# Performance work log

Hardware: AMD Instinct MI355X
Metric: run time of the kernel (lower is better)

The kernel has to match this reference:

```python
import jax, jax.numpy as jnp
import numpy as np

B, T, E, H = 8, 2048, 256, 8
D = E // H  # head_size = 32
EPS = 1e-5  # torch LayerNorm default


def _layernorm(x, g, b):
    m = jnp.mean(x, axis=-1, keepdims=True)
    v = jnp.var(x, axis=-1, keepdims=True)
    return (x - m) / jnp.sqrt(v + EPS) * g + b


def setup_inputs() -> dict:
    key = jax.random.key(0)
    ks = jax.random.split(key, 9)
    s = lambda k, shape, fan: (jax.random.normal(k, shape, jnp.float32) / np.sqrt(fan)).astype(jnp.float32)
    return {
        "x": jax.random.normal(ks[0], (B, T, E), jnp.float32),
        "wq": s(ks[1], (H, E, D), E),
        "wk": s(ks[2], (H, E, D), E),
        "wv": s(ks[3], (H, E, D), E),
        "w_lin": s(ks[4], (E, E), E),
        "b_lin": jnp.zeros((E,), jnp.float32),
        "g1": jnp.ones((E,), jnp.float32),
        "beta1": jnp.zeros((E,), jnp.float32),
        "g2": jnp.ones((E,), jnp.float32),
        "beta2": jnp.zeros((E,), jnp.float32),
        "w_f1": s(ks[5], (E, 4 * E), E),
        "b_f1": jnp.zeros((4 * E,), jnp.float32),
        "w_f2": s(ks[6], (4 * E, E), 4 * E),
        "b_f2": jnp.zeros((E,), jnp.float32),
    }


def reference(x, wq, wk, wv, w_lin, b_lin, g1, beta1, g2, beta2, w_f1, b_f1, w_f2, b_f2):
    b, t, e = x.shape
    xn = _layernorm(x, g1, beta1)  # norm1
    # all heads at once: (B,T,E) x (H,E,D) -> (B,H,T,D)
    q = jnp.einsum('bte,hed->bhtd', xn, wq)
    k = jnp.einsum('bte,hed->bhtd', xn, wk)
    v = jnp.einsum('bte,hed->bhtd', xn, wv)
    # scale uses C = embedding_size (as in source, not head_size)
    scores = jnp.einsum('bhtd,bhsd->bhts', q, k) * (e ** -0.5)
    mask = jnp.tril(jnp.ones((t, t), bool))  # (query t, key s)
    scores = jnp.where(mask[None, None, :, :], scores, -jnp.inf)
    # source applies softmax over dim=1 of (B,T,T) = the QUERY axis -> axis 2 of bhts
    attn = jax.nn.softmax(scores, axis=2)
    heads = jnp.einsum('bhts,bhsd->bhtd', attn, v)
    heads = heads.transpose(0, 2, 1, 3).reshape(b, t, e)  # concat over heads
    xh = xn + heads  # residual around attention
    xl = xh @ w_lin + b_lin  # projection (dropout is identity at eval)
    x2 = _layernorm(xl, g2, beta2)  # norm2
    ff = jax.nn.relu(x2 @ w_f1 + b_f1) @ w_f2 + b_f2  # FFN (dropout identity)
    return x2 + ff
```

## Files before the change

### kernel.cpp

```cpp
#include <hip/hip_runtime.h>
#include <math.h>

#define TT 2048
#define TE 256
#define NTOK 16384
#define QSCALE (0.0625f * 1.44269504088896f)

typedef short  bf16x8 __attribute__((ext_vector_type(8)));
typedef float  f32x4  __attribute__((ext_vector_type(4)));
typedef float  f32x16 __attribute__((ext_vector_type(16)));
typedef unsigned short u16x4 __attribute__((ext_vector_type(4)));
typedef unsigned short u16x8 __attribute__((ext_vector_type(8)));

__device__ __forceinline__ unsigned short f2b(float f) {
    union { float f; unsigned int u; } v; v.f = f;
    unsigned int r = v.u + 0x7FFF + ((v.u >> 16) & 1);
    return (unsigned short)(r >> 16);
}
__device__ __forceinline__ float b2f(unsigned short u) {
    union { unsigned int i; float f; } v; v.i = ((unsigned int)u) << 16;
    return v.f;
}
#if __has_builtin(__builtin_amdgcn_cvt_pk_bf16_f32)
__device__ __forceinline__ unsigned int pk_bf16(float a, float b) {
    typedef __bf16 bf2 __attribute__((ext_vector_type(2)));
    union { bf2 v; unsigned int u; } u;
    u.v = __builtin_amdgcn_cvt_pk_bf16_f32(a, b);
    return u.u;
}
#else
__device__ __forceinline__ unsigned int pk_bf16(float a, float b) {
    return (unsigned int)f2b(a) | ((unsigned int)f2b(b) << 16);
}
#endif
#if __has_builtin(__builtin_amdgcn_exp2f)
#define FEXP2(x) __builtin_amdgcn_exp2f(x)
#else
#define FEXP2(x) __expf(0.69314718056f * (x))
#endif
__device__ __forceinline__ void pswap(unsigned &a, unsigned &b) {
#if __has_builtin(__builtin_amdgcn_permlane32_swap)
    auto r = __builtin_amdgcn_permlane32_swap(a, b, false, false);
    a = r[0]; b = r[1];
#else
    asm("v_permlane32_swap_b32 %0, %1" : "+v"(a), "+v"(b));
#endif
}
__device__ __forceinline__ bf16x8 ld8(const unsigned short* p) {
    return *(const bf16x8*)p;
}
__device__ __forceinline__ void gl_lds16(const unsigned short* g, unsigned short* l) {
    __builtin_amdgcn_global_load_lds(
        (const __attribute__((address_space(1))) unsigned int*)(uintptr_t)g,
        (__attribute__((address_space(3))) unsigned int*)(uintptr_t)l,
        16, 0, 0);
}
#define MFMA16(a, b, c) __builtin_amdgcn_mfma_f32_16x16x32_bf16((a), (b), (c), 0, 0, 0)
#define MFMA32(a, b, c) __builtin_amdgcn_mfma_f32_32x32x16_bf16((a), (b), (c), 0, 0, 0)


__global__ __launch_bounds__(256) void conv_w(const float* __restrict__ wq,
                                              const float* __restrict__ wk,
                                              const float* __restrict__ wv,
                                              const float* __restrict__ w_lin,
                                              const float* __restrict__ w_f1,
                                              const float* __restrict__ w_f2,
                                              unsigned short* __restrict__ Wqkv,
                                              unsigned short* __restrict__ Wlin,
                                              unsigned short* __restrict__ Wf1,
                                              unsigned short* __restrict__ Wf2) {
    int idx = blockIdx.x * 256 + threadIdx.x;
    if (idx < 196608) {
        int n = idx >> 8, k = idx & 255;
        int which = n >> 8, h = (n >> 5) & 7, d = n & 31;
        const float* w = (which == 0) ? wq : (which == 1) ? wk : wv;
        Wqkv[idx] = f2b(w[(h * 256 + k) * 32 + d]);
    } else if (idx < 262144) {
        int i = idx - 196608; int n = i >> 8, k = i & 255;
        Wlin[i] = f2b(w_lin[k * 256 + n]);
    } else if (idx < 524288) {
        int i = idx - 262144; int n = i >> 8, k = i & 255;
        Wf1[i] = f2b(w_f1[k * 1024 + n]);
    } else {
        int i = idx - 524288; int n = i >> 10, k = i & 1023;
        Wf2[i] = f2b(w_f2[k * 256 + n]);
    }
}

__global__ __launch_bounds__(256) void ln_w(const float* __restrict__ X,
                                            const float* __restrict__ g,
                                            const float* __restrict__ bta,
                                            float* __restrict__ Y,
                                            unsigned short* __restrict__ Yb) {
    int row = blockIdx.x * 4 + (threadIdx.x >> 6);
    int lane = threadIdx.x & 63;
    const float4 v = *(const float4*)&X[(size_t)row * TE + lane * 4];
    float s = v.x + v.y + v.z + v.w;
    float s2 = v.x * v.x + v.y * v.y + v.z * v.z + v.w * v.w;
#pragma unroll
    for (int off = 1; off <= 32; off <<= 1) {
        s  += __shfl_xor(s,  off, 64);
        s2 += __shfl_xor(s2, off, 64);
    }
    float mean = s * (1.0f / TE);
    float var = s2 * (1.0f / TE) - mean * mean;
    float rstd = rsqrtf(var + 1e-5f);
    const float4 gg = *(const float4*)&g[lane * 4];
    const float4 bb = *(const float4*)&bta[lane * 4];
    float4 o;
    o.x = (v.x - mean) * rstd * gg.x + bb.x;
    o.y = (v.y - mean) * rstd * gg.y + bb.y;
    o.z = (v.z - mean) * rstd * gg.z + bb.z;
    o.w = (v.w - mean) * rstd * gg.w + bb.w;
    if (Y) *(float4*)&Y[(size_t)row * TE + lane * 4] = o;
    if (Yb) {
        u16x4 ob = { f2b(o.x), f2b(o.y), f2b(o.z), f2b(o.w) };
        *(u16x4*)&Yb[(size_t)row * TE + lane * 4] = ob;
    }
}

__global__ __launch_bounds__(256) void ln2_red(const float* __restrict__ Pp,
                                               const float* __restrict__ bias,
                                               const float* __restrict__ g,
                                               const float* __restrict__ bta,
                                               unsigned short* __restrict__ Yb) {
    const size_t SL = (size_t)NTOK * TE;
    int row = blockIdx.x * 4 + (threadIdx.x >> 6);
    int lane = threadIdx.x & 63;
    size_t base = (size_t)row * TE + lane * 4;
    const float4 p0 = *(const float4*)&Pp[base];
    const float4 p1 = *(const float4*)&Pp[SL + base];
    const float4 bl = *(const float4*)&bias[lane * 4];
    float4 v;
    v.x = p0.x + p1.x + bl.x; v.y = p0.y + p1.y + bl.y;
    v.z = p0.z + p1.z + bl.z; v.w = p0.w + p1.w + bl.w;
    float s = v.x + v.y + v.z + v.w;
    float s2 = v.x * v.x + v.y * v.y + v.z * v.z + v.w * v.w;
#pragma unroll
    for (int off = 1; off <= 32; off <<= 1) {
        s  += __shfl_xor(s,  off, 64);
        s2 += __shfl_xor(s2, off, 64);
    }
    float mean = s * (1.0f / TE);
    float var = s2 * (1.0f / TE) - mean * mean;
    float rstd = rsqrtf(var + 1e-5f);
    const float4 gg = *(const float4*)&g[lane * 4];
    const float4 bb = *(const float4*)&bta[lane * 4];
    u16x4 ob = { f2b((v.x - mean) * rstd * gg.x + bb.x),
                 f2b((v.y - mean) * rstd * gg.y + bb.y),
                 f2b((v.z - mean) * rstd * gg.z + bb.z),
                 f2b((v.w - mean) * rstd * gg.w + bb.w) };
    *(u16x4*)&Yb[base] = ob;
}

__global__ __launch_bounds__(256) void reduce2(const unsigned short* __restrict__ Pf,
                                               const float* __restrict__ bias,
                                               const unsigned short* __restrict__ x2b,
                                               float* __restrict__ out) {
    const size_t SL = (size_t)NTOK * TE;
    int row = blockIdx.x * 4 + (threadIdx.x >> 6);
    int lane = threadIdx.x & 63;
    size_t base = (size_t)row * TE + lane * 4;
    const float4 bl = *(const float4*)&bias[lane * 4];
    u16x4 r = *(const u16x4*)&x2b[base];
    float4 acc;
    acc.x = bl.x + b2f(r[0]); acc.y = bl.y + b2f(r[1]);
    acc.z = bl.z + b2f(r[2]); acc.w = bl.w + b2f(r[3]);
#pragma unroll
    for (int z = 0; z < 4; ++z) {
        u16x4 p = *(const u16x4*)&Pf[z * SL + base];
        acc.x += b2f(p[0]); acc.y += b2f(p[1]);
        acc.z += b2f(p[2]); acc.w += b2f(p[3]);
    }
    *(float4*)&out[base] = acc;
}

template<int KS>
__global__ __launch_bounds__(256) void gemm_lds(const unsigned short* __restrict__ A,
                                                int lda,
                                                const unsigned short* __restrict__ Bt,
                                                int ldb,
                                                const float* __restrict__ bias,
                                                float* __restrict__ outF,
                                                unsigned short* __restrict__ outB,
                                                int N, int relu) {
    __shared__ unsigned short Al[2][128 * 32];
    __shared__ unsigned short Bl[2][128 * 32];
    int tid = threadIdx.x;
    int w = tid >> 6, lane = tid & 63, q = lane >> 4, col = lane & 15;
    int wm = w & 1, wn = w >> 1;
    int m0 = blockIdx.x * 128;
    int n0 = blockIdx.y * 128;
    int koff = blockIdx.z * KS;
    size_t zoff = (size_t)blockIdx.z * NTOK * N;
    f32x4 acc[4][4] = {};
    int srow = lane >> 2;
    int skq  = ((lane & 3) ^ ((srow >> 1) & 3)) * 8;
    const unsigned short* Ag0 = A  + (size_t)(m0 + w * 32 + srow) * lda + koff + skq;
    const unsigned short* Ag1 = Ag0 + (size_t)16 * lda;
    const unsigned short* Bg0 = Bt + (size_t)(n0 + w * 32 + srow) * ldb + koff + skq;
    const unsigned short* Bg1 = Bg0 + (size_t)16 * ldb;
    int rq = (q ^ ((col >> 1) & 3)) * 8;
#define G_STAGE(cur, k0) do { \
        gl_lds16(Ag0 + (k0), &Al[cur][(w * 32) * 32]); \
        gl_lds16(Ag1 + (k0), &Al[cur][(w * 32 + 16) * 32]); \
        gl_lds16(Bg0 + (k0), &Bl[cur][(w * 32) * 32]); \
        gl_lds16(Bg1 + (k0), &Bl[cur][(w * 32 + 16) * 32]); \
    } while (0)
    G_STAGE(0, 0);
    __syncthreads();
    int cur = 0;
#pragma unroll
    for (int k0 = 0; k0 < KS; k0 += 32) {
        int kn = k0 + 32;
        if (kn < KS) G_STAGE(cur ^ 1, kn);
        bf16x8 a[4], b[4];
#pragma unroll
        for (int i = 0; i < 4; ++i)
            a[i] = ld8(&Al[cur][(wm * 64 + i * 16 + col) * 32 + rq]);
#pragma unroll
        for (int j = 0; j < 4; ++j)
            b[j] = ld8(&Bl[cur][(wn * 64 + j * 16 + col) * 32 + rq]);
#pragma unroll
        for (int i = 0; i < 4; ++i)
#pragma unroll
            for (int j = 0; j < 4; ++j)
                acc[i][j] = MFMA16(a[i], b[j], acc[i][j]);
        if (kn < KS) { __syncthreads(); cur ^= 1; }
    }
#undef G_STAGE
#pragma unroll
    for (int i = 0; i < 4; ++i)
#pragma unroll
    for (int j = 0; j < 4; ++j) {
        int n = n0 + wn * 64 + j * 16 + col;
#pragma unroll
        for (int r = 0; r < 4; ++r) {
            int m = m0 + wm * 64 + i * 16 + q * 4 + r;
            float v = acc[i][j][r];
            if (bias) v += bias[n];
            if (relu) v = fmaxf(v, 0.f);
            if (outF) outF[zoff + (size_t)m * N + n] = v;
            if (outB) outB[zoff + (size_t)m * N + n] = f2b(v);
        }
    }
}

__global__ __launch_bounds__(256) void gemm_qkv(const unsigned short* __restrict__ A,
                                                const unsigned short* __restrict__ Bt,
                                                unsigned short* __restrict__ Qd,
                                                unsigned short* __restrict__ Kd,
                                                unsigned short* __restrict__ Vc) {
    const int K = 256;
    __shared__ unsigned short Al[2][128 * 32];
    __shared__ unsigned short Bl[2][128 * 32];
    int tid = threadIdx.x;
    int w = tid >> 6, lane = tid & 63, q = lane >> 4, col = lane & 15;
    int wm = w & 1, wn = w >> 1;
    int m0 = blockIdx.x * 128;
    int n0 = blockIdx.y * 128;
    f32x4 acc[4][4] = {};
    int srow = lane >> 2;
    int skq  = ((lane & 3) ^ ((srow >> 1) & 3)) * 8;
    const unsigned short* Ag0 = A  + (size_t)(m0 + w * 32 + srow) * K + skq;
    const unsigned short* Ag1 = Ag0 + (size_t)16 * K;
    const unsigned short* Bg0 = Bt + (size_t)(n0 + w * 32 + srow) * K + skq;
    const unsigned short* Bg1 = Bg0 + (size_t)16 * K;
    int rq = (q ^ ((col >> 1) & 3)) * 8;
#define G_STAGE(cur, k0) do { \
        gl_lds16(Ag0 + (k0), &Al[cur][(w * 32) * 32]); \
        gl_lds16(Ag1 + (k0), &Al[cur][(w * 32 + 16) * 32]); \
        gl_lds16(Bg0 + (k0), &Bl[cur][(w * 32) * 32]); \
        gl_lds16(Bg1 + (k0), &Bl[cur][(w * 32 + 16) * 32]); \
    } while (0)
    G_STAGE(0, 0);
    __syncthreads();
    int cur = 0;
#pragma unroll
    for (int k0 = 0; k0 < K; k0 += 32) {
        int kn = k0 + 32;
        if (kn < K) G_STAGE(cur ^ 1, kn);
        bf16x8 a[4], b[4];
#pragma unroll
        for (int i = 0; i < 4; ++i)
            a[i] = ld8(&Al[cur][(wm * 64 + i * 16 + col) * 32 + rq]);
#pragma unroll
        for (int j = 0; j < 4; ++j)
            b[j] = ld8(&Bl[cur][(wn * 64 + j * 16 + col) * 32 + rq]);
#pragma unroll
        for (int i = 0; i < 4; ++i)
#pragma unroll
            for (int j = 0; j < 4; ++j)
                acc[i][j] = MFMA16(a[i], b[j], acc[i][j]);
        if (kn < K) { __syncthreads(); cur ^= 1; }
    }
#undef G_STAGE
#pragma unroll
    for (int i = 0; i < 4; ++i)
#pragma unroll
    for (int j = 0; j < 4; ++j) {
        int n = n0 + wn * 64 + j * 16 + col;
        int which = n >> 8, h = (n >> 5) & 7, d = n & 31;
        int m = m0 + wm * 64 + i * 16 + q * 4;
        int b = m >> 11, t = m & 2047;
        int bh = b * 8 + h;
        if (which == 0) {
            size_t qb = ((size_t)(bh * 2 + (d >> 4)) * TT + t) * 16 + (d & 15);
#pragma unroll
            for (int r = 0; r < 4; ++r)
                Qd[qb + r * 16] = f2b(acc[i][j][r] * QSCALE);
        } else if (which == 1) {
            size_t kb = ((size_t)(bh * 2 + (d >> 4)) * TT + t) * 16 + (d & 15);
#pragma unroll
            for (int r = 0; r < 4; ++r)
                Kd[kb + r * 16] = f2b(acc[i][j][r]);
        } else {
            uint2 pv;
            pv.x = pk_bf16(acc[i][j][0], acc[i][j][1]);
            pv.y = pk_bf16(acc[i][j][2], acc[i][j][3]);
            *(uint2*)&Vc[(((size_t)bh * 256 + (t >> 3)) * 32 + d) * 8 + (t & 7)] = pv;
        }
    }
}

__global__ __launch_bounds__(256, 4) void attn_cols(const unsigned short* __restrict__ Qd,
                                                    const unsigned short* __restrict__ Kd,
                                                    float* __restrict__ colLinv) {
    __shared__ float Lb[4][32];
    int tid = threadIdx.x;
    int w = tid >> 6, lane = tid & 63, hi = lane >> 5, l31 = lane & 31;
    int bh = blockIdx.x;
    int u = blockIdx.y;
    const unsigned short* Qb = Qd + ((size_t)bh * 2 * TT + l31) * 16 + hi * 8;
    const unsigned short* Kb = Kd + ((size_t)bh * 2 * TT + l31) * 16 + hi * 8;
    const f32x16 z16 = {};
#pragma unroll
    for (int phase = 0; phase < 2; ++phase) {
        int stile = phase ? (63 - u) : u;
        int sbase = stile * 32;
        bf16x8 a0 = ld8(Kb + (size_t)sbase * 16);
        bf16x8 a1 = ld8(Kb + ((size_t)TT + sbase) * 16);
        float acc[16] = {};
        for (int ct = stile + w; ct < 64; ct += 4) {
            int t0 = ct * 32;
            bf16x8 q0 = ld8(Qb + (size_t)t0 * 16);
            bf16x8 q1 = ld8(Qb + ((size_t)TT + t0) * 16);
            f32x16 st = MFMA32(a0, q0, z16);
            st = MFMA32(a1, q1, st);
            if (ct == stile) {
#pragma unroll
                for (int r = 0; r < 16; ++r) {
                    int s_local = (r & 3) + 8 * (r >> 2) + 4 * hi;
                    acc[r] += (l31 >= s_local) ? FEXP2(st[r]) : 0.f;
                }
            } else {
#pragma unroll
                for (int r = 0; r < 16; ++r) acc[r] += FEXP2(st[r]);
            }
        }
#pragma unroll
        for (int off = 1; off <= 16; off <<= 1)
#pragma unroll
            for (int r = 0; r < 16; ++r) acc[r] += __shfl_xor(acc[r], off, 64);
        if (l31 == 0) {
#pragma unroll
            for (int r = 0; r < 16; ++r) {
                int s_local = (r & 3) + 8 * (r >> 2) + 4 * hi;
                Lb[w][s_local] = acc[r];
            }
        }
        __syncthreads();
        if (tid < 32) {
            float s = Lb[0][tid] + Lb[1][tid] + Lb[2][tid] + Lb[3][tid];
            colLinv[(size_t)bh * TT + sbase + tid] = 1.0f / s;
        }
        __syncthreads();
    }
}

__global__ __launch_bounds__(256) void scale_vt(unsigned short* __restrict__ Vc,
                                                const float* __restrict__ colLinv) {
    int bh = blockIdx.x >> 5, g = blockIdx.x & 31;
    int sb = g * 8 + (threadIdx.x >> 5);
    int d = threadIdx.x & 31;
    size_t base = (((size_t)bh * 256 + sb) * 32 + d) * 8;
    u16x8 v = *(const u16x8*)&Vc[base];
    const float4 i0 = *(const float4*)&colLinv[(size_t)bh * TT + sb * 8];
    const float4 i1 = *(const float4*)&colLinv[(size_t)bh * TT + sb * 8 + 4];
    u16x8 o;
    o[0] = f2b(b2f(v[0]) * i0.x); o[1] = f2b(b2f(v[1]) * i0.y);
    o[2] = f2b(b2f(v[2]) * i0.z); o[3] = f2b(b2f(v[3]) * i0.w);
    o[4] = f2b(b2f(v[4]) * i1.x); o[5] = f2b(b2f(v[5]) * i1.y);
    o[6] = f2b(b2f(v[6]) * i1.z); o[7] = f2b(b2f(v[7]) * i1.w);
    *(u16x8*)&Vc[base] = o;
}

__global__ __launch_bounds__(256, 4) void attn_out(const unsigned short* __restrict__ Qd,
                                                   const unsigned short* __restrict__ Kd,
                                                   const unsigned short* __restrict__ Vc,
                                                   const unsigned short* __restrict__ xnb,
                                                   unsigned short* __restrict__ xh_bf) {
    __shared__ float Ob[4][32][36];
    int tid = threadIdx.x;
    int w = tid >> 6, lane = tid & 63, hi = lane >> 5, l31 = lane & 31;
    int bh = blockIdx.x, b = bh >> 3, h = bh & 7;
    int u = blockIdx.y;
    const unsigned short* Kb = Kd + ((size_t)bh * 2 * TT + l31) * 16 + hi * 8;
    const unsigned short* Vb = Vc + (size_t)bh * 65536 + hi * 256 + l31 * 8;
    const unsigned short* Qbase = Qd + ((size_t)bh * 2 * TT + l31) * 16 + hi * 8;
    const f32x16 z16 = {};

#pragma unroll
    for (int phase = 0; phase < 2; ++phase) {
        int tt = phase ? (63 - u) : u;
        int tbase = tt * 32;
        bf16x8 q0 = ld8(Qbase + (size_t)tbase * 16);
        bf16x8 q1 = ld8(Qbase + ((size_t)TT + tbase) * 16);
        f32x16 acc = z16;

        int c = w;
        bf16x8 ka0 = ld8(Kb + (size_t)c * 512);
        bf16x8 ka1 = ld8(Kb + (size_t)TT * 16 + (size_t)c * 512);
        bf16x8 vv0 = ld8(Vb + (size_t)c * 1024);
        bf16x8 vv1 = ld8(Vb + (size_t)c * 1024 + 512);

        for (; c <= tt; c += 4) {
            bool diag = (c == tt);
            f32x16 st = MFMA32(ka0, q0, z16);
            st = MFMA32(ka1, q1, st);
            int cn = c + 4;
            if (cn <= tt) {
                ka0 = ld8(Kb + (size_t)cn * 512);
                ka1 = ld8(Kb + (size_t)TT * 16 + (size_t)cn * 512);
            }
            unsigned Wd[8];
            if (diag) {
#pragma unroll
                for (int j = 0; j < 8; ++j) {
                    int r0 = 2 * j;
                    int s0 = (r0 & 3) + 8 * (r0 >> 2) + 4 * hi;
                    float e0 = (s0 <= l31)     ? FEXP2(st[r0])     : 0.f;
                    float e1 = (s0 + 1 <= l31) ? FEXP2(st[r0 + 1]) : 0.f;
                    Wd[j] = pk_bf16(e0, e1);
                }
            } else {
#pragma unroll
                for (int j = 0; j < 8; ++j)
                    Wd[j] = pk_bf16(FEXP2(st[2 * j]), FEXP2(st[2 * j + 1]));
            }
            pswap(Wd[0], Wd[2]); pswap(Wd[1], Wd[3]);
            pswap(Wd[4], Wd[6]); pswap(Wd[5], Wd[7]);
            union { unsigned u4[4]; bf16x8 v; } pa0, pa1;
            pa0.u4[0] = Wd[0]; pa0.u4[1] = Wd[1]; pa0.u4[2] = Wd[2]; pa0.u4[3] = Wd[3];
            pa1.u4[0] = Wd[4]; pa1.u4[1] = Wd[5]; pa1.u4[2] = Wd[6]; pa1.u4[3] = Wd[7];
            acc = MFMA32(pa0.v, vv0, acc);
            acc = MFMA32(pa1.v, vv1, acc);
            if (cn <= tt) {
                vv0 = ld8(Vb + (size_t)cn * 1024);
                vv1 = ld8(Vb + (size_t)cn * 1024 + 512);
            }
        }

#pragma unroll
        for (int r = 0; r < 16; ++r) {
            int t = (r & 3) + 8 * (r >> 2) + 4 * hi;
            Ob[w][t][l31] = acc[r];
        }
        __syncthreads();
        {
            int row = tid >> 3;
            int c4 = (tid & 7) * 4;
            float4 s0 = *(const float4*)&Ob[0][row][c4];
            float4 s1 = *(const float4*)&Ob[1][row][c4];
            float4 s2 = *(const float4*)&Ob[2][row][c4];
            float4 s3 = *(const float4*)&Ob[3][row][c4];
            size_t base = ((size_t)(b * TT) + tbase + row) * TE + h * 32 + c4;
            u16x4 xv = *(const u16x4*)&xnb[base];
            u16x4 ob = { f2b(s0.x + s1.x + s2.x + s3.x + b2f(xv[0])),
                         f2b(s0.y + s1.y + s2.y + s3.y + b2f(xv[1])),
                         f2b(s0.z + s1.z + s2.z + s3.z + b2f(xv[2])),
                         f2b(s0.w + s1.w + s2.w + s3.w + b2f(xv[3])) };
            *(u16x4*)&xh_bf[base] = ob;
        }
        __syncthreads();
    }
}

extern "C" void kernel_launch(void* const* d_in, const int* in_sizes, int n_in,
                              void* d_out, int out_size, void* d_ws, size_t ws_size,
                              hipStream_t stream) {
    (void)in_sizes; (void)n_in; (void)out_size; (void)ws_size;
    const float* x     = (const float*)d_in[0];
    const float* wq    = (const float*)d_in[1];
    const float* wk    = (const float*)d_in[2];
    const float* wv    = (const float*)d_in[3];
    const float* w_lin = (const float*)d_in[4];
    const float* b_lin = (const float*)d_in[5];
    const float* g1    = (const float*)d_in[6];
    const float* beta1 = (const float*)d_in[7];
    const float* g2    = (const float*)d_in[8];
    const float* beta2 = (const float*)d_in[9];
    const float* w_f1  = (const float*)d_in[10];
    const float* b_f1  = (const float*)d_in[11];
    const float* w_f2  = (const float*)d_in[12];
    const float* b_f2  = (const float*)d_in[13];
    float* out = (float*)d_out;

    char* ws = (char*)d_ws;
    unsigned short* Wqkv_t = (unsigned short*)(ws + 0);
    unsigned short* Wlin_t = (unsigned short*)(ws + 393216);
    unsigned short* Wf1_t  = (unsigned short*)(ws + 524288);
    unsigned short* Wf2_t  = (unsigned short*)(ws + 1048576);
    float*          colLinv= (float*)(ws + 1572864);
    unsigned short* xn_bf  = (unsigned short*)(ws + 2097152);
    unsigned short* Qbf    = (unsigned short*)(ws + 10485760);
    unsigned short* Kbf    = (unsigned short*)(ws + 18874368);
    unsigned short* Vt     = (unsigned short*)(ws + 27262976);
    unsigned short* xh_bf  = (unsigned short*)(ws + 35651584);
    float*          Pp     = (float*)(ws + 44040192);
    unsigned short* Pf     = (unsigned short*)(ws + 44040192);
    unsigned short* x2_bf  = xn_bf;
    unsigned short* h_bf   = Qbf;

    conv_w<<<3072, 256, 0, stream>>>(wq, wk, wv, w_lin, w_f1, w_f2,
                                     Wqkv_t, Wlin_t, Wf1_t, Wf2_t);
    ln_w<<<4096, 256, 0, stream>>>(x, g1, beta1, nullptr, xn_bf);
    gemm_qkv<<<dim3(128, 6), 256, 0, stream>>>(xn_bf, Wqkv_t, Qbf, Kbf, Vt);
    attn_cols<<<dim3(64, 32), 256, 0, stream>>>(Qbf, Kbf, colLinv);
    scale_vt<<<2048, 256, 0, stream>>>(Vt, colLinv);
    attn_out<<<dim3(64, 32), 256, 0, stream>>>(Qbf, Kbf, Vt, xn_bf, xh_bf);
    gemm_lds<128><<<dim3(128, 2, 2), 256, 0, stream>>>(xh_bf, 256, Wlin_t, 256,
                                                       nullptr, Pp, nullptr, 256, 0);
    ln2_red<<<4096, 256, 0, stream>>>(Pp, b_lin, g2, beta2, x2_bf);
    gemm_lds<256><<<dim3(128, 8, 1), 256, 0, stream>>>(x2_bf, 256, Wf1_t, 256,
                                                       b_f1, nullptr, h_bf, 1024, 1);
    gemm_lds<256><<<dim3(128, 2, 4), 256, 0, stream>>>(h_bf, 1024, Wf2_t, 1024,
                                                       nullptr, nullptr, Pf, 256, 0);
    reduce2<<<4096, 256, 0, stream>>>(Pf, b_f2, x2_bf, out);
}
```

Baseline: 262.8 us.

## Fuse prep kernels, fold V scaling into attn_cols, triple-buffer GEMMs, stage epilogue

Merges weight conversion and the first LayerNorm into one launch, and folds the per-column V scaling into attn_cols so the scale_vt kernel and the colLinv buffer go away. The GEMM main loops move from double to triple-buffered LDS with explicit vmcnt waits and a single barrier per step. The gemm_lds epilogue is staged through LDS so outputs go out as vector stores. This cuts launch count and intermediate traffic and improves load/compute overlap, at the cost of more LDS per block and hand-written wait counts that rely on the number of outstanding loads being exact.

```diff
diff --git a/kernel.cpp b/kernel.cpp
--- a/kernel.cpp
+++ b/kernel.cpp
@@ -59,16 +59,43 @@
 #define MFMA32(a, b, c) __builtin_amdgcn_mfma_f32_32x32x16_bf16((a), (b), (c), 0, 0, 0)
 
 
-__global__ __launch_bounds__(256) void conv_w(const float* __restrict__ wq,
-                                              const float* __restrict__ wk,
-                                              const float* __restrict__ wv,
-                                              const float* __restrict__ w_lin,
-                                              const float* __restrict__ w_f1,
-                                              const float* __restrict__ w_f2,
-                                              unsigned short* __restrict__ Wqkv,
-                                              unsigned short* __restrict__ Wlin,
-                                              unsigned short* __restrict__ Wf1,
-                                              unsigned short* __restrict__ Wf2) {
+__global__ __launch_bounds__(256) void prep(const float* __restrict__ wq,
+                                            const float* __restrict__ wk,
+                                            const float* __restrict__ wv,
+                                            const float* __restrict__ w_lin,
+                                            const float* __restrict__ w_f1,
+                                            const float* __restrict__ w_f2,
+                                            unsigned short* __restrict__ Wqkv,
+                                            unsigned short* __restrict__ Wlin,
+                                            unsigned short* __restrict__ Wf1,
+                                            unsigned short* __restrict__ Wf2,
+                                            const float* __restrict__ X,
+                                            const float* __restrict__ g,
+                                            const float* __restrict__ bta,
+                                            unsigned short* __restrict__ Yb) {
+    if (blockIdx.x >= 3072) {
+        int row = (blockIdx.x - 3072) * 4 + (threadIdx.x >> 6);
+        int lane = threadIdx.x & 63;
+        const float4 v = *(const float4*)&X[(size_t)row * TE + lane * 4];
+        float s = v.x + v.y + v.z + v.w;
+        float s2 = v.x * v.x + v.y * v.y + v.z * v.z + v.w * v.w;
+#pragma unroll
+        for (int off = 1; off <= 32; off <<= 1) {
+            s  += __shfl_xor(s,  off, 64);
+            s2 += __shfl_xor(s2, off, 64);
+        }
+        float mean = s * (1.0f / TE);
+        float var = s2 * (1.0f / TE) - mean * mean;
+        float rstd = rsqrtf(var + 1e-5f);
+        const float4 gg = *(const float4*)&g[lane * 4];
+        const float4 bb = *(const float4*)&bta[lane * 4];
+        u16x4 ob = { f2b((v.x - mean) * rstd * gg.x + bb.x),
+                     f2b((v.y - mean) * rstd * gg.y + bb.y),
+                     f2b((v.z - mean) * rstd * gg.z + bb.z),
+                     f2b((v.w - mean) * rstd * gg.w + bb.w) };
+        *(u16x4*)&Yb[(size_t)row * TE + lane * 4] = ob;
+        return;
+    }
     int idx = blockIdx.x * 256 + threadIdx.x;
     if (idx < 196608) {
         int n = idx >> 8, k = idx & 255;
@@ -84,38 +111,6 @@
     } else {
         int i = idx - 524288; int n = i >> 10, k = i & 1023;
         Wf2[i] = f2b(w_f2[k * 256 + n]);
-    }
-}
-
-__global__ __launch_bounds__(256) void ln_w(const float* __restrict__ X,
-                                            const float* __restrict__ g,
-                                            const float* __restrict__ bta,
-                                            float* __restrict__ Y,
-                                            unsigned short* __restrict__ Yb) {
-    int row = blockIdx.x * 4 + (threadIdx.x >> 6);
-    int lane = threadIdx.x & 63;
-    const float4 v = *(const float4*)&X[(size_t)row * TE + lane * 4];
-    float s = v.x + v.y + v.z + v.w;
-    float s2 = v.x * v.x + v.y * v.y + v.z * v.z + v.w * v.w;
-#pragma unroll
-    for (int off = 1; off <= 32; off <<= 1) {
-        s  += __shfl_xor(s,  off, 64);
-        s2 += __shfl_xor(s2, off, 64);
-    }
-    float mean = s * (1.0f / TE);
-    float var = s2 * (1.0f / TE) - mean * mean;
-    float rstd = rsqrtf(var + 1e-5f);
-    const float4 gg = *(const float4*)&g[lane * 4];
-    const float4 bb = *(const float4*)&bta[lane * 4];
-    float4 o;
-    o.x = (v.x - mean) * rstd * gg.x + bb.x;
-    o.y = (v.y - mean) * rstd * gg.y + bb.y;
-    o.z = (v.z - mean) * rstd * gg.z + bb.z;
-    o.w = (v.w - mean) * rstd * gg.w + bb.w;
-    if (Y) *(float4*)&Y[(size_t)row * TE + lane * 4] = o;
-    if (Yb) {
-        u16x4 ob = { f2b(o.x), f2b(o.y), f2b(o.z), f2b(o.w) };
-        *(u16x4*)&Yb[(size_t)row * TE + lane * 4] = ob;
     }
 }
 
@@ -184,8 +179,8 @@
                                                 float* __restrict__ outF,
                                                 unsigned short* __restrict__ outB,
                                                 int N, int relu) {
-    __shared__ unsigned short Al[2][128 * 32];
-    __shared__ unsigned short Bl[2][128 * 32];
+    __shared__ unsigned short Al[3][128 * 32];
+    __shared__ unsigned short Bl[3][128 * 32];
     int tid = threadIdx.x;
     int w = tid >> 6, lane = tid & 63, q = lane >> 4, col = lane & 15;
     int wm = w & 1, wn = w >> 1;
@@ -201,47 +196,78 @@
     const unsigned short* Bg0 = Bt + (size_t)(n0 + w * 32 + srow) * ldb + koff + skq;
     const unsigned short* Bg1 = Bg0 + (size_t)16 * ldb;
     int rq = (q ^ ((col >> 1) & 3)) * 8;
-#define G_STAGE(cur, k0) do { \
-        gl_lds16(Ag0 + (k0), &Al[cur][(w * 32) * 32]); \
-        gl_lds16(Ag1 + (k0), &Al[cur][(w * 32 + 16) * 32]); \
-        gl_lds16(Bg0 + (k0), &Bl[cur][(w * 32) * 32]); \
-        gl_lds16(Bg1 + (k0), &Bl[cur][(w * 32 + 16) * 32]); \
+#define G_STAGE(bf, kk) do { \
+        gl_lds16(Ag0 + (kk), &Al[bf][(w * 32) * 32]); \
+        gl_lds16(Ag1 + (kk), &Al[bf][(w * 32 + 16) * 32]); \
+        gl_lds16(Bg0 + (kk), &Bl[bf][(w * 32) * 32]); \
+        gl_lds16(Bg1 + (kk), &Bl[bf][(w * 32 + 16) * 32]); \
     } while (0)
     G_STAGE(0, 0);
-    __syncthreads();
-    int cur = 0;
+    G_STAGE(1, 32);
 #pragma unroll
     for (int k0 = 0; k0 < KS; k0 += 32) {
-        int kn = k0 + 32;
-        if (kn < KS) G_STAGE(cur ^ 1, kn);
+        const int jb = (k0 >> 5) % 3;
+        if (k0 + 32 < KS) { asm volatile("s_waitcnt vmcnt(4)" ::: "memory"); }
+        else              { asm volatile("s_waitcnt vmcnt(0)" ::: "memory"); }
+        __builtin_amdgcn_s_barrier();
+        if (k0 + 64 < KS) G_STAGE((jb + 2) % 3, k0 + 64);
         bf16x8 a[4], b[4];
 #pragma unroll
         for (int i = 0; i < 4; ++i)
-            a[i] = ld8(&Al[cur][(wm * 64 + i * 16 + col) * 32 + rq]);
+            a[i] = ld8(&Al[jb][(wm * 64 + i * 16 + col) * 32 + rq]);
 #pragma unroll
         for (int j = 0; j < 4; ++j)
-            b[j] = ld8(&Bl[cur][(wn * 64 + j * 16 + col) * 32 + rq]);
+            b[j] = ld8(&Bl[jb][(wn * 64 + j * 16 + col) * 32 + rq]);
 #pragma unroll
         for (int i = 0; i < 4; ++i)
 #pragma unroll
             for (int j = 0; j < 4; ++j)
                 acc[i][j] = MFMA16(a[i], b[j], acc[i][j]);
-        if (kn < KS) { __syncthreads(); cur ^= 1; }
+        __builtin_amdgcn_sched_barrier(0);
     }
 #undef G_STAGE
-#pragma unroll
-    for (int i = 0; i < 4; ++i)
-#pragma unroll
-    for (int j = 0; j < 4; ++j) {
-        int n = n0 + wn * 64 + j * 16 + col;
-#pragma unroll
-        for (int r = 0; r < 4; ++r) {
-            int m = m0 + wm * 64 + i * 16 + q * 4 + r;
-            float v = acc[i][j][r];
-            if (bias) v += bias[n];
-            if (relu) v = fmaxf(v, 0.f);
-            if (outF) outF[zoff + (size_t)m * N + n] = v;
-            if (outB) outB[zoff + (size_t)m * N + n] = f2b(v);
+    float* Cb = (float*)&Al[0][0];
+    const int CLD = 132;
+#pragma unroll
+    for (int i = 0; i < 4; ++i) {
+        __syncthreads();
+#pragma unroll
+        for (int j = 0; j < 4; ++j)
+#pragma unroll
+            for (int r = 0; r < 4; ++r)
+                Cb[(wm * 16 + q * 4 + r) * CLD + wn * 64 + j * 16 + col] = acc[i][j][r];
+        __syncthreads();
+        int row = tid >> 3;
+        int seg = (tid & 7) * 16;
+        int mloc = (row & 15) + i * 16 + (row >> 4) * 64;
+        int m = m0 + mloc;
+        int n = n0 + seg;
+        float vbuf[16];
+#pragma unroll
+        for (int u = 0; u < 16; ++u) vbuf[u] = Cb[row * CLD + seg + u];
+        if (bias) {
+#pragma unroll
+            for (int u4 = 0; u4 < 4; ++u4) {
+                float4 bb = *(const float4*)&bias[n + u4 * 4];
+                vbuf[u4 * 4 + 0] += bb.x; vbuf[u4 * 4 + 1] += bb.y;
+                vbuf[u4 * 4 + 2] += bb.z; vbuf[u4 * 4 + 3] += bb.w;
+            }
+        }
+        if (relu) {
+#pragma unroll
+            for (int u = 0; u < 16; ++u) vbuf[u] = fmaxf(vbuf[u], 0.f);
+        }
+        if (outF) {
+#pragma unroll
+            for (int u = 0; u < 16; u += 4)
+                *(float4*)&outF[zoff + (size_t)m * N + n + u] = *(const float4*)&vbuf[u];
+        }
+        if (outB) {
+            u16x8 o0, o1;
+#pragma unroll
+            for (int u = 0; u < 8; ++u) { o0[u] = f2b(vbuf[u]); o1[u] = f2b(vbuf[8 + u]); }
+            *(u16x8*)&outB[zoff + (size_t)m * N + n] = o0;
+            *(u16x8*)&outB[zoff + (size_t)m * N + n + 8] = o1;
         }
     }
 }
@@ -252,8 +278,8 @@
                                                 unsigned short* __restrict__ Kd,
                                                 unsigned short* __restrict__ Vc) {
     const int K = 256;
-    __shared__ unsigned short Al[2][128 * 32];
-    __shared__ unsigned short Bl[2][128 * 32];
+    __shared__ unsigned short Al[3][128 * 32];
+    __shared__ unsigned short Bl[3][128 * 32];
     int tid = threadIdx.x;
     int w = tid >> 6, lane = tid & 63, q = lane >> 4, col = lane & 15;
     int wm = w & 1, wn = w >> 1;
@@ -267,32 +293,34 @@
     const unsigned short* Bg0 = Bt + (size_t)(n0 + w * 32 + srow) * K + skq;
     const unsigned short* Bg1 = Bg0 + (size_t)16 * K;
     int rq = (q ^ ((col >> 1) & 3)) * 8;
-#define G_STAGE(cur, k0) do { \
-        gl_lds16(Ag0 + (k0), &Al[cur][(w * 32) * 32]); \
-        gl_lds16(Ag1 + (k0), &Al[cur][(w * 32 + 16) * 32]); \
-        gl_lds16(Bg0 + (k0), &Bl[cur][(w * 32) * 32]); \
-        gl_lds16(Bg1 + (k0), &Bl[cur][(w * 32 + 16) * 32]); \
+#define G_STAGE(bf, kk) do { \
+        gl_lds16(Ag0 + (kk), &Al[bf][(w * 32) * 32]); \
+        gl_lds16(Ag1 + (kk), &Al[bf][(w * 32 + 16) * 32]); \
+        gl_lds16(Bg0 + (kk), &Bl[bf][(w * 32) * 32]); \
+        gl_lds16(Bg1 + (kk), &Bl[bf][(w * 32 + 16) * 32]); \
     } while (0)
     G_STAGE(0, 0);
-    __syncthreads();
-    int cur = 0;
+    G_STAGE(1, 32);
 #pragma unroll
     for (int k0 = 0; k0 < K; k0 += 32) {
-        int kn = k0 + 32;
-        if (kn < K) G_STAGE(cur ^ 1, kn);
+        const int jb = (k0 >> 5) % 3;
+        if (k0 + 32 < K) { asm volatile("s_waitcnt vmcnt(4)" ::: "memory"); }
+        else             { asm volatile("s_waitcnt vmcnt(0)" ::: "memory"); }
+        __builtin_amdgcn_s_barrier();
+        if (k0 + 64 < K) G_STAGE((jb + 2) % 3, k0 + 64);
         bf16x8 a[4], b[4];
 #pragma unroll
         for (int i = 0; i < 4; ++i)
-            a[i] = ld8(&Al[cur][(wm * 64 + i * 16 + col) * 32 + rq]);
+            a[i] = ld8(&Al[jb][(wm * 64 + i * 16 + col) * 32 + rq]);
 #pragma unroll
         for (int j = 0; j < 4; ++j)
-            b[j] = ld8(&Bl[cur][(wn * 64 + j * 16 + col) * 32 + rq]);
+            b[j] = ld8(&Bl[jb][(wn * 64 + j * 16 + col) * 32 + rq]);
 #pragma unroll
         for (int i = 0; i < 4; ++i)
 #pragma unroll
             for (int j = 0; j < 4; ++j)
                 acc[i][j] = MFMA16(a[i], b[j], acc[i][j]);
-        if (kn < K) { __syncthreads(); cur ^= 1; }
+        __builtin_amdgcn_sched_barrier(0);
     }
 #undef G_STAGE
 #pragma unroll
@@ -325,8 +353,9 @@
 
 __global__ __launch_bounds__(256, 4) void attn_cols(const unsigned short* __restrict__ Qd,
                                                     const unsigned short* __restrict__ Kd,
-                                                    float* __restrict__ colLinv) {
+                                                    unsigned short* __restrict__ Vc) {
     __shared__ float Lb[4][32];
+    __shared__ float Linv[32];
     int tid = threadIdx.x;
     int w = tid >> 6, lane = tid & 63, hi = lane >> 5, l31 = lane & 31;
     int bh = blockIdx.x;
@@ -370,29 +399,21 @@
             }
         }
         __syncthreads();
-        if (tid < 32) {
-            float s = Lb[0][tid] + Lb[1][tid] + Lb[2][tid] + Lb[3][tid];
-            colLinv[(size_t)bh * TT + sbase + tid] = 1.0f / s;
-        }
-        __syncthreads();
-    }
-}
-
-__global__ __launch_bounds__(256) void scale_vt(unsigned short* __restrict__ Vc,
-                                                const float* __restrict__ colLinv) {
-    int bh = blockIdx.x >> 5, g = blockIdx.x & 31;
-    int sb = g * 8 + (threadIdx.x >> 5);
-    int d = threadIdx.x & 31;
-    size_t base = (((size_t)bh * 256 + sb) * 32 + d) * 8;
-    u16x8 v = *(const u16x8*)&Vc[base];
-    const float4 i0 = *(const float4*)&colLinv[(size_t)bh * TT + sb * 8];
-    const float4 i1 = *(const float4*)&colLinv[(size_t)bh * TT + sb * 8 + 4];
-    u16x8 o;
-    o[0] = f2b(b2f(v[0]) * i0.x); o[1] = f2b(b2f(v[1]) * i0.y);
-    o[2] = f2b(b2f(v[2]) * i0.z); o[3] = f2b(b2f(v[3]) * i0.w);
-    o[4] = f2b(b2f(v[4]) * i1.x); o[5] = f2b(b2f(v[5]) * i1.y);
-    o[6] = f2b(b2f(v[6]) * i1.z); o[7] = f2b(b2f(v[7]) * i1.w);
-    *(u16x8*)&Vc[base] = o;
+        if (tid < 32)
+            Linv[tid] = 1.0f / (Lb[0][tid] + Lb[1][tid] + Lb[2][tid] + Lb[3][tid]);
+        __syncthreads();
+        if (tid < 128) {
+            int sbl = tid >> 5;
+            int d = tid & 31;
+            size_t base = (((size_t)bh * 256 + stile * 4 + sbl) * 32 + d) * 8;
+            u16x8 v = *(const u16x8*)&Vc[base];
+            u16x8 o;
+#pragma unroll
+            for (int e = 0; e < 8; ++e) o[e] = f2b(b2f(v[e]) * Linv[sbl * 8 + e]);
+            *(u16x8*)&Vc[base] = o;
+        }
+        __syncthreads();
+    }
 }
 
 __global__ __launch_bounds__(256, 4) void attn_out(const unsigned short* __restrict__ Qd,
@@ -511,7 +532,6 @@
     unsigned short* Wlin_t = (unsigned short*)(ws + 393216);
     unsigned short* Wf1_t  = (unsigned short*)(ws + 524288);
     unsigned short* Wf2_t  = (unsigned short*)(ws + 1048576);
-    float*          colLinv= (float*)(ws + 1572864);
     unsigned short* xn_bf  = (unsigned short*)(ws + 2097152);
     unsigned short* Qbf    = (unsigned short*)(ws + 10485760);
     unsigned short* Kbf    = (unsigned short*)(ws + 18874368);
@@ -522,12 +542,11 @@
     unsigned short* x2_bf  = xn_bf;
     unsigned short* h_bf   = Qbf;
 
-    conv_w<<<3072, 256, 0, stream>>>(wq, wk, wv, w_lin, w_f1, w_f2,
-                                     Wqkv_t, Wlin_t, Wf1_t, Wf2_t);
-    ln_w<<<4096, 256, 0, stream>>>(x, g1, beta1, nullptr, xn_bf);
+    prep<<<7168, 256, 0, stream>>>(wq, wk, wv, w_lin, w_f1, w_f2,
+                                   Wqkv_t, Wlin_t, Wf1_t, Wf2_t,
+                                   x, g1, beta1, xn_bf);
     gemm_qkv<<<dim3(128, 6), 256, 0, stream>>>(xn_bf, Wqkv_t, Qbf, Kbf, Vt);
-    attn_cols<<<dim3(64, 32), 256, 0, stream>>>(Qbf, Kbf, colLinv);
-    scale_vt<<<2048, 256, 0, stream>>>(Vt, colLinv);
+    attn_cols<<<dim3(64, 32), 256, 0, stream>>>(Qbf, Kbf, Vt);
     attn_out<<<dim3(64, 32), 256, 0, stream>>>(Qbf, Kbf, Vt, xn_bf, xh_bf);
     gemm_lds<128><<<dim3(128, 2, 2), 256, 0, stream>>>(xh_bf, 256, Wlin_t, 256,
                                                        nullptr, Pp, nullptr, 256, 0);
```

Result: faster. 241.8 us (-8.0%).
